# Optimization experiments

Measured on AMD Instinct MI355X. Metric: run time of the kernel, lower is better.

## Reference

```python
import jax, jax.numpy as jnp
import numpy as np

ALPHA = 0.2  # LeakyReLU negative slope
NEG_BIG = -9e15


def setup_inputs() -> dict:
    key = jax.random.key(0)
    k_h, k_adj, k_W, k_a = jax.random.split(key, 4)
    B, N, F_in, F_out = 8, 2048, 128, 64
    h = jax.random.normal(k_h, (B, N, F_in), dtype=jnp.float32)
    adj = jax.random.randint(k_adj, (B, N, N), 0, 2, dtype=jnp.int32)
    # xavier_uniform: bound = sqrt(6/(fan_in+fan_out))
    bW = float(np.sqrt(6.0 / (F_in + F_out)))
    W = jax.random.uniform(k_W, (F_in, F_out), dtype=jnp.float32, minval=-bW, maxval=bW)
    ba = float(np.sqrt(6.0 / (2 * F_out + 1)))
    a = jax.random.uniform(k_a, (2 * F_out, 1), dtype=jnp.float32, minval=-ba, maxval=ba)
    return {"h": h, "adj": adj, "W": W, "a": a}


def reference(h, adj, W, a):
    # h: [B,N,Fin], adj: [B,N,N], W: [Fin,Fout], a: [2*Fout,1]
    F_out = W.shape[1]
    Wh = jnp.einsum('bnf,fo->bno', h, W)               # [B,N,Fout]
    a1 = a[:F_out, 0]                                   # [Fout] (source/i part)
    a2 = a[F_out:, 0]                                   # [Fout] (target/j part)
    # e_ij = leakyrelu(Wh_i . a1 + Wh_j . a2) -- avoids O(N^2*2F) concat
    si = Wh @ a1                                        # [B,N]
    sj = Wh @ a2                                        # [B,N]
    e = si[:, :, None] + sj[:, None, :]                 # [B,N,N]
    e = jnp.where(e > 0, e, ALPHA * e)                  # LeakyReLU
    e = jnp.where(adj > 0, e, NEG_BIG)                  # mask non-edges
    attention = jax.nn.softmax(e, axis=2)               # [B,N,N]
    # dropout omitted (eval / training=False)
    h_prime = jnp.einsum('bij,bjo->bio', attention, Wh)  # [B,N,Fout]
    return h_prime
```

## Files before the change

kernel.cpp:

```cpp
#include <hip/hip_runtime.h>
#include <hip/hip_bf16.h>

#define ALPHA 0.2f
#define LOG2E 1.4426950408889634f

typedef __attribute__((ext_vector_type(8))) short bf16x8;
typedef __attribute__((ext_vector_type(4))) float f32x4;
typedef __attribute__((ext_vector_type(4))) int i32x4;

__device__ __forceinline__ int cvt_pk_bf16(float lo, float hi) {
    int r;
    asm("v_cvt_pk_bf16_f32 %0, %1, %2" : "=v"(r) : "v"(lo), "v"(hi));
    return r;
}

__device__ __forceinline__ void stage16(const void* g, void* l) {
    __builtin_amdgcn_global_load_lds(
        (const __attribute__((address_space(1))) void*)g,
        (__attribute__((address_space(3))) void*)l, 16, 0, 0);
}

__global__ __launch_bounds__(256) void gat_precompute(
    const float* __restrict__ h, const float* __restrict__ W,
    const float* __restrict__ a, unsigned short* __restrict__ WhT,
    float* __restrict__ si2, float* __restrict__ sj2)
{
    __shared__ float h_lds[32][128];
    __shared__ float wh_lds[32][65];
    const int tid  = threadIdx.x;
    const int lane = tid & 63;
    const int wave = tid >> 6;
    const long long row0 = (long long)blockIdx.x * 32;

    {
        const float4* s4 = (const float4*)(h + row0 * 128);
        #pragma unroll
        for (int i = 0; i < 4; ++i) {
            int idx = tid + i * 256;
            float4 v = s4[idx];
            *(float4*)&h_lds[idx >> 5][(idx & 31) * 4] = v;
        }
    }
    __syncthreads();

    const float a1 = a[lane];
    const float a2 = a[64 + lane];
    float acc[8];
    #pragma unroll
    for (int r = 0; r < 8; ++r) acc[r] = 0.0f;

    for (int f = 0; f < 128; f += 4) {
        const float w0 = W[(f+0)*64 + lane];
        const float w1 = W[(f+1)*64 + lane];
        const float w2 = W[(f+2)*64 + lane];
        const float w3 = W[(f+3)*64 + lane];
        #pragma unroll
        for (int r = 0; r < 8; ++r) {
            const float4 hv = *(const float4*)&h_lds[wave*8 + r][f];
            acc[r] = fmaf(hv.x, w0, acc[r]);
            acc[r] = fmaf(hv.y, w1, acc[r]);
            acc[r] = fmaf(hv.z, w2, acc[r]);
            acc[r] = fmaf(hv.w, w3, acc[r]);
        }
    }

    #pragma unroll
    for (int r = 0; r < 8; ++r) {
        const int rr = wave*8 + r;
        wh_lds[rr][lane] = acc[r];
        float s1 = acc[r] * a1;
        float s2 = acc[r] * a2;
        #pragma unroll
        for (int off = 32; off > 0; off >>= 1) {
            s1 += __shfl_xor(s1, off);
            s2 += __shfl_xor(s2, off);
        }
        if (lane == 0) {
            si2[row0 + rr] = s1 * LOG2E;
            sj2[row0 + rr] = s2 * LOG2E;
        }
    }
    __syncthreads();

    const long long b  = row0 >> 11;
    const int n0 = (int)(row0 & 2047);
    const int o  = tid >> 2;
    const int c0 = (tid & 3) * 8;
    i32x4 pk;
    #pragma unroll
    for (int k = 0; k < 4; ++k)
        pk[k] = cvt_pk_bf16(wh_lds[c0 + 2*k][o], wh_lds[c0 + 2*k + 1][o]);
    *(i32x4*)(WhT + (b*64 + o)*2048 + n0 + c0) = pk;
}

__global__ __launch_bounds__(256) void gat_attention(
    const int* __restrict__ adj, const unsigned short* __restrict__ WhT,
    const float* __restrict__ si2, const float* __restrict__ sj2,
    float* __restrict__ out)
{
    __shared__ char ldsbuf[65536];
    const int tid  = threadIdx.x;
    const int lane = tid & 63;
    const int wave = tid >> 6;
    const int bid  = blockIdx.x;
    const int b    = bid >> 6;
    const int i0   = (bid & 63) << 5;
    const int arow = lane & 15;
    const int g    = lane >> 4;
    const int half = wave >> 1;
    const int rgrp = wave & 1;
    const long long bN = (long long)b * 2048;

    const int* asrc[4];
    #pragma unroll
    for (int rd = 0; rd < 4; ++rd) {
        int U = (wave*4 + rd)*64 + lane;
        int r = U >> 5, pu = U & 31;
        int u = pu ^ (r & 15);
        int col = (u < 16) ? u*4 : (1024 + (u-16)*4);
        asrc[rd] = adj + (bN + i0 + r)*2048 + col;
    }
    const unsigned short* wsrc[4];
    #pragma unroll
    for (int rd = 0; rd < 4; ++rd) {
        int U  = wave*256 + rd*64 + lane;
        int hf = U >> 9;
        int o  = (U & 511) >> 3;
        int pu = U & 7;
        wsrc[rd] = WhT + ((long long)b*64 + o)*2048 + hf*1024
                       + ((pu ^ (o & 7)) * 8);
    }

    const float* sjb = sj2 + bN;
    float mx = -INFINITY;
    #pragma unroll 4
    for (int i = 0; i < 32; ++i) mx = fmaxf(mx, sjb[lane + i*64]);
    #pragma unroll
    for (int off = 32; off > 0; off >>= 1) mx = fmaxf(mx, __shfl_xor(mx, off));

    const float si_r = si2[bN + i0 + rgrp*16 + arow];
    const float u0f  = si_r + mx;
    const float m2   = fmaxf(u0f, ALPHA * u0f);
    const float Ci   = si_r - m2;
    const float Di   = ALPHA * si_r - m2;
    const int   rr   = rgrp*16 + arow;

    f32x4 accf[4];
    #pragma unroll
    for (int ob = 0; ob < 4; ++ob) accf[ob] = (f32x4){0.f,0.f,0.f,0.f};
    f32x4 accl = (f32x4){0.f,0.f,0.f,0.f};
    bf16x8 ones;
    #pragma unroll
    for (int k = 0; k < 8; ++k) ones[k] = (short)0x3F80;

    #define STAGE(S, STEP) { \
        const int ja = (STEP) * 64; \
        char* ab_ = ldsbuf + (S)*32768; \
        stage16(asrc[0] + ja, ab_ + (wave*4+0)*1024); \
        stage16(asrc[1] + ja, ab_ + (wave*4+1)*1024); \
        stage16(asrc[2] + ja, ab_ + (wave*4+2)*1024); \
        stage16(asrc[3] + ja, ab_ + (wave*4+3)*1024); \
        char* wb_ = ldsbuf + (S)*32768 + 16384 + wave*4096; \
        stage16(wsrc[0] + ja, wb_ + 0*1024); \
        stage16(wsrc[1] + ja, wb_ + 1*1024); \
        stage16(wsrc[2] + ja, wb_ + 2*1024); \
        stage16(wsrc[3] + ja, wb_ + 3*1024); \
    }

    #define KKBODY(KK) { \
        const char* wb = ab + 16384 + half*8192; \
        const int ws = ((KK)*4 + g) ^ (arow & 7); \
        const bf16x8 bf0 = *(const bf16x8*)(wb + (( 0 + arow)*8 + ws)*16); \
        const bf16x8 bf1 = *(const bf16x8*)(wb + ((16 + arow)*8 + ws)*16); \
        const bf16x8 bf2 = *(const bf16x8*)(wb + ((32 + arow)*8 + ws)*16); \
        const bf16x8 bf3 = *(const bf16x8*)(wb + ((48 + arow)*8 + ws)*16); \
        const int u0a = half*16 + (KK)*8 + g*2; \
        const i32x4 A0 = *(const i32x4*)(ab + rr*512 + ((u0a    ) ^ arow)*16); \
        const i32x4 A1 = *(const i32x4*)(ab + rr*512 + ((u0a + 1) ^ arow)*16); \
        const float* sjp = sjb + half*1024 + j0 + (KK)*32 + g*8; \
        const f32x4 S0 = *(const f32x4*)(sjp); \
        const f32x4 S1 = *(const f32x4*)(sjp + 4); \
        float p[8]; \
        _Pragma("unroll") \
        for (int e = 0; e < 4; ++e) { \
            float pe = __builtin_amdgcn_exp2f( \
                fmaxf(Ci + S0[e], fmaf(ALPHA, S0[e], Di))); \
            p[e] = (A0[e] > 0) ? pe : 0.0f; \
        } \
        _Pragma("unroll") \
        for (int e = 0; e < 4; ++e) { \
            float pe = __builtin_amdgcn_exp2f( \
                fmaxf(Ci + S1[e], fmaf(ALPHA, S1[e], Di))); \
            p[4+e] = (A1[e] > 0) ? pe : 0.0f; \
        } \
        i32x4 pk_; \
        pk_[0] = cvt_pk_bf16(p[0], p[1]); \
        pk_[1] = cvt_pk_bf16(p[2], p[3]); \
        pk_[2] = cvt_pk_bf16(p[4], p[5]); \
        pk_[3] = cvt_pk_bf16(p[6], p[7]); \
        const bf16x8 pa = __builtin_bit_cast(bf16x8, pk_); \
        accl    = __builtin_amdgcn_mfma_f32_16x16x32_bf16(pa, ones, accl, 0, 0, 0); \
        accf[0] = __builtin_amdgcn_mfma_f32_16x16x32_bf16(pa, bf0, accf[0], 0, 0, 0); \
        accf[1] = __builtin_amdgcn_mfma_f32_16x16x32_bf16(pa, bf1, accf[1], 0, 0, 0); \
        accf[2] = __builtin_amdgcn_mfma_f32_16x16x32_bf16(pa, bf2, accf[2], 0, 0, 0); \
        accf[3] = __builtin_amdgcn_mfma_f32_16x16x32_bf16(pa, bf3, accf[3], 0, 0, 0); \
    }

    STAGE(0, 0);
    __syncthreads();

    int s = 0;
    for (int st = 0; st < 16; ++st) {
        if (st < 15) STAGE(s^1, st+1);
        const char* ab = ldsbuf + s*32768;
        const int j0 = st * 64;
        KKBODY(0);
        KKBODY(1);
        __syncthreads();
        s ^= 1;
    }

    float* accb = (float*)ldsbuf;
    float* lb   = (float*)(ldsbuf + 16384);
    #pragma unroll
    for (int ob = 0; ob < 4; ++ob)
        #pragma unroll
        for (int rg2 = 0; rg2 < 4; ++rg2)
            accb[(wave*16 + g*4 + rg2)*64 + ob*16 + arow] = accf[ob][rg2];
    if (arow == 0) {
        #pragma unroll
        for (int rg2 = 0; rg2 < 4; ++rg2)
            lb[wave*16 + g*4 + rg2] = accl[rg2];
    }
    __syncthreads();

    const int r  = tid >> 3;
    const int o0 = (tid & 7) * 8;
    const int rg = r >> 4, rl = r & 15;
    const float L   = lb[rg*16 + rl] + lb[(rg+2)*16 + rl];
    const float inv = 1.0f / L;
    float ov[8];
    #pragma unroll
    for (int k = 0; k < 8; ++k)
        ov[k] = (accb[(rg*16 + rl)*64 + o0 + k]
               + accb[((rg+2)*16 + rl)*64 + o0 + k]) * inv;
    float* op = out + (bN + i0 + r)*64 + o0;
    *(float4*)op       = (float4){ov[0], ov[1], ov[2], ov[3]};
    *(float4*)(op + 4) = (float4){ov[4], ov[5], ov[6], ov[7]};
}

extern "C" void kernel_launch(void* const* d_in, const int* in_sizes, int n_in,
                              void* d_out, int out_size, void* d_ws, size_t ws_size,
                              hipStream_t stream) {
    const float* h   = (const float*)d_in[0];
    const int*   adj = (const int*)d_in[1];
    const float* W   = (const float*)d_in[2];
    const float* a   = (const float*)d_in[3];
    float* out = (float*)d_out;

    unsigned short* WhT = (unsigned short*)d_ws;
    float* si2 = (float*)((char*)d_ws + (size_t)16384*64*2);
    float* sj2 = si2 + 16384;

    gat_precompute<<<512, 256, 0, stream>>>(h, W, a, WhT, si2, sj2);
    gat_attention<<<512, 256, 0, stream>>>(adj, WhT, si2, sj2, out);
}
```

Baseline: 48.24 us.

## Pre-swizzle Wh into MFMA fragment layout and shrink attention tiles to 16 rows

The precompute kernel now writes Wh in the exact bf16 MFMA B-fragment order, so the attention kernel loads B operands straight from global memory into registers (software double-buffered) instead of staging them through LDS. The attention tile drops from 32 to 16 query rows across 1024 blocks, with each wave taking a quarter of the j range and the partial sums reduced through LDS at the end. The LDS footprint shrinks from 64KB to about 16KB and launch bounds request 4 blocks per CU, aiming at higher occupancy and less LDS traffic. In exchange, each Wh fragment is read by twice as many blocks, and the direct global loads of B may expose latency.

```diff
diff --git a/kernel.cpp b/kernel.cpp
--- a/kernel.cpp
+++ b/kernel.cpp
@@ -22,7 +22,7 @@
 
 __global__ __launch_bounds__(256) void gat_precompute(
     const float* __restrict__ h, const float* __restrict__ W,
-    const float* __restrict__ a, unsigned short* __restrict__ WhT,
+    const float* __restrict__ a, unsigned short* __restrict__ WhF,
     float* __restrict__ si2, float* __restrict__ sj2)
 {
     __shared__ float h_lds[32][128];
@@ -83,53 +83,47 @@
     __syncthreads();
 
     const long long b  = row0 >> 11;
-    const int n0 = (int)(row0 & 2047);
-    const int o  = tid >> 2;
-    const int c0 = (tid & 3) * 8;
+    const int jcb  = (int)((row0 & 2047) >> 5);
+    const int ob   = tid >> 6;
+    const int ln   = tid & 63;
+    const int ar   = ln & 15;
+    const int gg   = ln >> 4;
     i32x4 pk;
     #pragma unroll
     for (int k = 0; k < 4; ++k)
-        pk[k] = cvt_pk_bf16(wh_lds[c0 + 2*k][o], wh_lds[c0 + 2*k + 1][o]);
-    *(i32x4*)(WhT + (b*64 + o)*2048 + n0 + c0) = pk;
-}
-
-__global__ __launch_bounds__(256) void gat_attention(
-    const int* __restrict__ adj, const unsigned short* __restrict__ WhT,
+        pk[k] = cvt_pk_bf16(wh_lds[gg*8 + 2*k    ][ob*16 + ar],
+                            wh_lds[gg*8 + 2*k + 1][ob*16 + ar]);
+    *(i32x4*)(WhF + ((b*64 + jcb)*4 + ob)*512 + ln*8) = pk;
+}
+
+__global__ __launch_bounds__(256, 4) void gat_attention(
+    const int* __restrict__ adj, const unsigned short* __restrict__ WhF,
     const float* __restrict__ si2, const float* __restrict__ sj2,
     float* __restrict__ out)
 {
-    __shared__ char ldsbuf[65536];
+    __shared__ char ldsbuf[16640];
     const int tid  = threadIdx.x;
     const int lane = tid & 63;
     const int wave = tid >> 6;
-    const int bid  = blockIdx.x;
-    const int b    = bid >> 6;
-    const int i0   = (bid & 63) << 5;
+    const int b    = blockIdx.x & 7;
+    const int i0   = (int)((blockIdx.x >> 3) << 4);
     const int arow = lane & 15;
     const int g    = lane >> 4;
-    const int half = wave >> 1;
-    const int rgrp = wave & 1;
     const long long bN = (long long)b * 2048;
 
-    const int* asrc[4];
-    #pragma unroll
-    for (int rd = 0; rd < 4; ++rd) {
-        int U = (wave*4 + rd)*64 + lane;
-        int r = U >> 5, pu = U & 31;
-        int u = pu ^ (r & 15);
-        int col = (u < 16) ? u*4 : (1024 + (u-16)*4);
-        asrc[rd] = adj + (bN + i0 + r)*2048 + col;
-    }
-    const unsigned short* wsrc[4];
-    #pragma unroll
-    for (int rd = 0; rd < 4; ++rd) {
-        int U  = wave*256 + rd*64 + lane;
-        int hf = U >> 9;
-        int o  = (U & 511) >> 3;
-        int pu = U & 7;
-        wsrc[rd] = WhT + ((long long)b*64 + o)*2048 + hf*1024
-                       + ((pu ^ (o & 7)) * 8);
-    }
+    const int* asrc0;
+    const int* asrc1;
+    {
+        int r = lane >> 3;
+        int u = (lane & 7) ^ (r & 7);
+        asrc0 = adj + (bN + i0 + r)*2048 + wave*512 + u*4;
+        int r2 = 8 + (lane >> 3);
+        int u2 = (lane & 7) ^ (r2 & 7);
+        asrc1 = adj + (bN + i0 + r2)*2048 + wave*512 + u2*4;
+    }
+
+    const unsigned short* fbase =
+        WhF + ((long long)(b*64 + wave*16) * 4) * 512 + lane*8;
 
     const float* sjb = sj2 + bN;
     float mx = -INFINITY;
@@ -138,12 +132,13 @@
     #pragma unroll
     for (int off = 32; off > 0; off >>= 1) mx = fmaxf(mx, __shfl_xor(mx, off));
 
-    const float si_r = si2[bN + i0 + rgrp*16 + arow];
+    const float si_r = si2[bN + i0 + arow];
     const float u0f  = si_r + mx;
     const float m2   = fmaxf(u0f, ALPHA * u0f);
     const float Ci   = si_r - m2;
     const float Di   = ALPHA * si_r - m2;
-    const int   rr   = rgrp*16 + arow;
+
+    const float* sjq = sjb + wave*512 + g*8;
 
     f32x4 accf[4];
     #pragma unroll
@@ -153,33 +148,27 @@
     #pragma unroll
     for (int k = 0; k < 8; ++k) ones[k] = (short)0x3F80;
 
+    bf16x8 cb0, cb1, cb2, cb3, nb0, nb1, nb2, nb3;
+
     #define STAGE(S, STEP) { \
-        const int ja = (STEP) * 64; \
-        char* ab_ = ldsbuf + (S)*32768; \
-        stage16(asrc[0] + ja, ab_ + (wave*4+0)*1024); \
-        stage16(asrc[1] + ja, ab_ + (wave*4+1)*1024); \
-        stage16(asrc[2] + ja, ab_ + (wave*4+2)*1024); \
-        stage16(asrc[3] + ja, ab_ + (wave*4+3)*1024); \
-        char* wb_ = ldsbuf + (S)*32768 + 16384 + wave*4096; \
-        stage16(wsrc[0] + ja, wb_ + 0*1024); \
-        stage16(wsrc[1] + ja, wb_ + 1*1024); \
-        stage16(wsrc[2] + ja, wb_ + 2*1024); \
-        stage16(wsrc[3] + ja, wb_ + 3*1024); \
-    }
-
-    #define KKBODY(KK) { \
-        const char* wb = ab + 16384 + half*8192; \
-        const int ws = ((KK)*4 + g) ^ (arow & 7); \
-        const bf16x8 bf0 = *(const bf16x8*)(wb + (( 0 + arow)*8 + ws)*16); \
-        const bf16x8 bf1 = *(const bf16x8*)(wb + ((16 + arow)*8 + ws)*16); \
-        const bf16x8 bf2 = *(const bf16x8*)(wb + ((32 + arow)*8 + ws)*16); \
-        const bf16x8 bf3 = *(const bf16x8*)(wb + ((48 + arow)*8 + ws)*16); \
-        const int u0a = half*16 + (KK)*8 + g*2; \
-        const i32x4 A0 = *(const i32x4*)(ab + rr*512 + ((u0a    ) ^ arow)*16); \
-        const i32x4 A1 = *(const i32x4*)(ab + rr*512 + ((u0a + 1) ^ arow)*16); \
-        const float* sjp = sjb + half*1024 + j0 + (KK)*32 + g*8; \
-        const f32x4 S0 = *(const f32x4*)(sjp); \
-        const f32x4 S1 = *(const f32x4*)(sjp + 4); \
+        char* base_ = ldsbuf + (S)*8192 + wave*2048; \
+        stage16(asrc0 + (STEP)*32, base_); \
+        stage16(asrc1 + (STEP)*32, base_ + 1024); \
+    }
+
+    #define LOADB(D0, D1, D2, D3, STEP) { \
+        D0 = *(const bf16x8*)(fbase + ((STEP)*4 + 0)*512); \
+        D1 = *(const bf16x8*)(fbase + ((STEP)*4 + 1)*512); \
+        D2 = *(const bf16x8*)(fbase + ((STEP)*4 + 2)*512); \
+        D3 = *(const bf16x8*)(fbase + ((STEP)*4 + 3)*512); \
+    }
+
+    #define BODY(S, STEP) { \
+        const char* ab = ldsbuf + (S)*8192 + wave*2048; \
+        const i32x4 A0 = *(const i32x4*)(ab + arow*128 + ((g*2    ) ^ (arow & 7))*16); \
+        const i32x4 A1 = *(const i32x4*)(ab + arow*128 + ((g*2 + 1) ^ (arow & 7))*16); \
+        const f32x4 S0 = *(const f32x4*)(sjq + (STEP)*32); \
+        const f32x4 S1 = *(const f32x4*)(sjq + (STEP)*32 + 4); \
         float p[8]; \
         _Pragma("unroll") \
         for (int e = 0; e < 4; ++e) { \
@@ -199,54 +188,57 @@
         pk_[2] = cvt_pk_bf16(p[4], p[5]); \
         pk_[3] = cvt_pk_bf16(p[6], p[7]); \
         const bf16x8 pa = __builtin_bit_cast(bf16x8, pk_); \
-        accl    = __builtin_amdgcn_mfma_f32_16x16x32_bf16(pa, ones, accl, 0, 0, 0); \
-        accf[0] = __builtin_amdgcn_mfma_f32_16x16x32_bf16(pa, bf0, accf[0], 0, 0, 0); \
-        accf[1] = __builtin_amdgcn_mfma_f32_16x16x32_bf16(pa, bf1, accf[1], 0, 0, 0); \
-        accf[2] = __builtin_amdgcn_mfma_f32_16x16x32_bf16(pa, bf2, accf[2], 0, 0, 0); \
-        accf[3] = __builtin_amdgcn_mfma_f32_16x16x32_bf16(pa, bf3, accf[3], 0, 0, 0); \
+        accl    = __builtin_amdgcn_mfma_f32_16x16x32_bf16(pa, ones, accl,    0, 0, 0); \
+        accf[0] = __builtin_amdgcn_mfma_f32_16x16x32_bf16(pa, cb0, accf[0], 0, 0, 0); \
+        accf[1] = __builtin_amdgcn_mfma_f32_16x16x32_bf16(pa, cb1, accf[1], 0, 0, 0); \
+        accf[2] = __builtin_amdgcn_mfma_f32_16x16x32_bf16(pa, cb2, accf[2], 0, 0, 0); \
+        accf[3] = __builtin_amdgcn_mfma_f32_16x16x32_bf16(pa, cb3, accf[3], 0, 0, 0); \
     }
 
     STAGE(0, 0);
+    LOADB(cb0, cb1, cb2, cb3, 0);
     __syncthreads();
 
     int s = 0;
-    for (int st = 0; st < 16; ++st) {
-        if (st < 15) STAGE(s^1, st+1);
-        const char* ab = ldsbuf + s*32768;
-        const int j0 = st * 64;
-        KKBODY(0);
-        KKBODY(1);
+    for (int st = 0; st < 15; ++st) {
+        STAGE(s^1, st+1);
+        LOADB(nb0, nb1, nb2, nb3, st+1);
+        BODY(s, st);
         __syncthreads();
+        cb0 = nb0; cb1 = nb1; cb2 = nb2; cb3 = nb3;
         s ^= 1;
     }
-
+    BODY(s, 15);
+
+    __syncthreads();
     float* accb = (float*)ldsbuf;
     float* lb   = (float*)(ldsbuf + 16384);
     #pragma unroll
     for (int ob = 0; ob < 4; ++ob)
         #pragma unroll
-        for (int rg2 = 0; rg2 < 4; ++rg2)
-            accb[(wave*16 + g*4 + rg2)*64 + ob*16 + arow] = accf[ob][rg2];
+        for (int reg = 0; reg < 4; ++reg)
+            accb[(wave*16 + g*4 + reg)*64 + ob*16 + arow] = accf[ob][reg];
     if (arow == 0) {
         #pragma unroll
-        for (int rg2 = 0; rg2 < 4; ++rg2)
-            lb[wave*16 + g*4 + rg2] = accl[rg2];
-    }
-    __syncthreads();
-
-    const int r  = tid >> 3;
-    const int o0 = (tid & 7) * 8;
-    const int rg = r >> 4, rl = r & 15;
-    const float L   = lb[rg*16 + rl] + lb[(rg+2)*16 + rl];
+        for (int reg = 0; reg < 4; ++reg)
+            lb[wave*16 + g*4 + reg] = accl[reg];
+    }
+    __syncthreads();
+
+    const int r  = tid >> 4;
+    const int c0 = (tid & 15) * 4;
+    const float L = lb[r] + lb[16 + r] + lb[32 + r] + lb[48 + r];
     const float inv = 1.0f / L;
-    float ov[8];
-    #pragma unroll
-    for (int k = 0; k < 8; ++k)
-        ov[k] = (accb[(rg*16 + rl)*64 + o0 + k]
-               + accb[((rg+2)*16 + rl)*64 + o0 + k]) * inv;
-    float* op = out + (bN + i0 + r)*64 + o0;
-    *(float4*)op       = (float4){ov[0], ov[1], ov[2], ov[3]};
-    *(float4*)(op + 4) = (float4){ov[4], ov[5], ov[6], ov[7]};
+    float4 v;
+    v.x = (accb[r*64 + c0 + 0] + accb[(16+r)*64 + c0 + 0]
+         + accb[(32+r)*64 + c0 + 0] + accb[(48+r)*64 + c0 + 0]) * inv;
+    v.y = (accb[r*64 + c0 + 1] + accb[(16+r)*64 + c0 + 1]
+         + accb[(32+r)*64 + c0 + 1] + accb[(48+r)*64 + c0 + 1]) * inv;
+    v.z = (accb[r*64 + c0 + 2] + accb[(16+r)*64 + c0 + 2]
+         + accb[(32+r)*64 + c0 + 2] + accb[(48+r)*64 + c0 + 2]) * inv;
+    v.w = (accb[r*64 + c0 + 3] + accb[(16+r)*64 + c0 + 3]
+         + accb[(32+r)*64 + c0 + 3] + accb[(48+r)*64 + c0 + 3]) * inv;
+    *(float4*)(out + (bN + i0 + r)*64 + c0) = v;
 }
 
 extern "C" void kernel_launch(void* const* d_in, const int* in_sizes, int n_in,
@@ -258,10 +250,10 @@
     const float* a   = (const float*)d_in[3];
     float* out = (float*)d_out;
 
-    unsigned short* WhT = (unsigned short*)d_ws;
+    unsigned short* WhF = (unsigned short*)d_ws;
     float* si2 = (float*)((char*)d_ws + (size_t)16384*64*2);
     float* sj2 = si2 + 16384;
 
-    gat_precompute<<<512, 256, 0, stream>>>(h, W, a, WhT, si2, sj2);
-    gat_attention<<<512, 256, 0, stream>>>(adj, WhT, si2, sj2, out);
-}
+    gat_precompute<<<512, 256, 0, stream>>>(h, W, a, WhF, si2, sj2);
+    gat_attention<<<1024, 256, 0, stream>>>(adj, WhF, si2, sj2, out);
+}
```

Result: faster. 45.22 us (-6.3%).
